# Kernel optimization log

Hardware: AMD Instinct MI355X
Metric: run time of the kernel (lower is better)

Reference implementation:

```python
import jax, jax.numpy as jnp
import numpy as np

MODEL_DIM = 256
NUM_HEADS = 4
HEAD_DIM = MODEL_DIM // NUM_HEADS
MAX_LEN = 512
EPS = 1e-5


def positional_embedding(n, dim):
    pos = jnp.arange(n, dtype=jnp.float32)[:, None]
    div = jnp.exp(jnp.arange(0, dim, 2, dtype=jnp.float32) * (-np.log(10000.0) / dim))
    pe = jnp.zeros((n, dim), dtype=jnp.float32)
    pe = pe.at[:, 0::2].set(jnp.sin(pos * div))
    pe = pe.at[:, 1::2].set(jnp.cos(pos * div))
    return pe


def layer_norm(x, g, b):
    mu = jnp.mean(x, axis=-1, keepdims=True)
    var = jnp.mean(jnp.square(x - mu), axis=-1, keepdims=True)
    return (x - mu) * jax.lax.rsqrt(var + EPS) * g + b


def setup_inputs() -> dict:
    key = jax.random.key(0)
    ks = jax.random.split(key, 20)
    B, N = 64, 512
    d = MODEL_DIM

    def lin(k, fan_in, fan_out):
        lim = 1.0 / np.sqrt(fan_in)
        return jax.random.uniform(k, (fan_out, fan_in), jnp.float32, -lim, lim)

    def xavier(k, fan_in, fan_out):
        lim = np.sqrt(6.0 / (fan_in + fan_out))
        return jax.random.uniform(k, (fan_out, fan_in), jnp.float32, -lim, lim)

    return {
        "x": jax.random.normal(ks[0], (B, N, 769), jnp.float32),
        "y": jax.random.normal(ks[1], (B, N, 674), jnp.float32),
        "z": jnp.zeros((B, 1), jnp.float32),
        "Wr": lin(ks[2], 769, d), "br": jnp.zeros((d,), jnp.float32),
        "Wf": lin(ks[3], 674, d), "bf": jnp.zeros((d,), jnp.float32),
        "g_x": jnp.ones((d,), jnp.float32), "b_x": jnp.zeros((d,), jnp.float32),
        "g_y": jnp.ones((d,), jnp.float32), "b_y": jnp.zeros((d,), jnp.float32),
        "Wq": xavier(ks[4], d, d), "bq": jnp.zeros((d,), jnp.float32),
        "Wk": xavier(ks[5], d, d), "bk": jnp.zeros((d,), jnp.float32),
        "Wv": xavier(ks[6], d, d), "bv": jnp.zeros((d,), jnp.float32),
        "Wo": xavier(ks[7], d, d), "bo": jnp.zeros((d,), jnp.float32),
        "g_m": jnp.ones((d,), jnp.float32), "b_m": jnp.zeros((d,), jnp.float32),
        "W1": lin(ks[8], d, d), "b1": jnp.zeros((d,), jnp.float32),
        "W2": lin(ks[9], d, d), "b2": jnp.zeros((d,), jnp.float32),
        "Wc": lin(ks[10], d, 2), "bc": jnp.zeros((2,), jnp.float32),
    }


def reference(x, y, z, Wr, br, Wf, bf, g_x, b_x, g_y, b_y,
              Wq, bq, Wk, bk, Wv, bv, Wo, bo, g_m, b_m,
              W1, b1, W2, b2, Wc, bc):
    B, N, _ = x.shape
    d, H, hd = MODEL_DIM, NUM_HEADS, HEAD_DIM
    pe = positional_embedding(MAX_LEN, d)[:N]  # (N, d)

    xp = layer_norm(x @ Wr.T + br + pe[None], g_x, b_x)  # (B,N,d)
    yp = layer_norm(y @ Wf.T + bf + pe[None], g_y, b_y)

    # cross-attention (non-causal, no masks, eval-mode dropout)
    q = (xp @ Wq.T + bq).reshape(B, N, H, hd)
    k = (yp @ Wk.T + bk).reshape(B, N, H, hd)
    v = (yp @ Wv.T + bv).reshape(B, N, H, hd)
    scale = hd ** -0.5
    scores = jnp.einsum("bshd,bthd->bhst", q, k) * scale  # (B,H,N,N)
    attn = jax.nn.softmax(scores, axis=-1)
    ctx = jnp.einsum("bhst,bthd->bshd", attn, v).reshape(B, N, d)
    attn_out = ctx @ Wo.T + bo

    x_res = layer_norm(xp + attn_out, g_m, b_m)
    mlp = jax.nn.relu(x_res @ W1.T + b1) @ W2.T + b2
    x_mlp = x_res + mlp
    pooled = jnp.mean(x_mlp, axis=1)  # (B,d)
    logits = pooled @ Wc.T + bc  # (B,2)
    return logits
```

## Files before the change

### kernel.cpp

```cpp
#include <hip/hip_runtime.h>
#include <hip/hip_bf16.h>

#define B_   64
#define N_   512
#define D_   256
#define H_   4
#define HD_  64

typedef __hip_bfloat16 bf16;
typedef __attribute__((ext_vector_type(8))) short short8;
typedef __attribute__((ext_vector_type(4))) float floatx4;

__device__ __forceinline__ float bf2f(bf16 v) { return __bfloat162float(v); }
__device__ __forceinline__ unsigned short f2us(float f) {
    bf16 h = __float2bfloat16(f);
    union { bf16 h; unsigned short u; } c; c.h = h; return c.u;
}

typedef __attribute__((address_space(1))) const unsigned int asg_u32;
typedef __attribute__((address_space(3))) unsigned int asl_u32;
__device__ __forceinline__ void gl_lds16(const void* g, void* l) {
    __builtin_amdgcn_global_load_lds((asg_u32*)g, (asl_u32*)l, 16, 0, 0);
}

__global__ __launch_bounds__(256)
void convw_k(const float* __restrict__ Wr, const float* __restrict__ Wf,
             const float* __restrict__ Wq, const float* __restrict__ Wk,
             const float* __restrict__ Wv, const float* __restrict__ Wo,
             const float* __restrict__ W1, const float* __restrict__ W2,
             bf16* __restrict__ dst)
{
    const int seg = blockIdx.y;
    const float* src; int Kreal, Kp; size_t off;
    switch (seg) {
        case 0: src = Wr; Kreal = 769; Kp = 800; off = 0; break;
        case 1: src = Wf; Kreal = 674; Kp = 704; off = 256 * 800; break;
        default:
            src = (seg == 2) ? Wq : (seg == 3) ? Wk : (seg == 4) ? Wv
                : (seg == 5) ? Wo : (seg == 6) ? W1 : W2;
            Kreal = 256; Kp = 256;
            off = 256 * 800 + 256 * 704 + (size_t)(seg - 2) * 256 * 256;
            break;
    }
    const int idx = blockIdx.x * 256 + threadIdx.x;
    if (idx >= 256 * Kp / 8) return;
    const int rowk = idx * 8;
    const int n = rowk / Kp, k0 = rowk % Kp;
    unsigned short tmp[8];
    #pragma unroll
    for (int j = 0; j < 8; ++j) {
        int kk = k0 + j;
        tmp[j] = f2us(kk < Kreal ? src[(size_t)n * Kreal + kk] : 0.f);
    }
    *(short8*)&dst[off + (size_t)rowk] = *(short8*)tmp;
}

__global__ __launch_bounds__(256)
void pe_k(float* __restrict__ pe)
{
    const int n = blockIdx.x, c = threadIdx.x;
    const int j = c & ~1;
    float freq = __expf(-(float)j * (9.210340371976184f / 256.0f));
    float ang = (float)n * freq;
    pe[n * 256 + c] = (c & 1) ? cosf(ang) : sinf(ang);
}

template<bool F32A>
__global__ __launch_bounds__(256)
void gemm_rp_t(const bf16* __restrict__ A, const float* __restrict__ A32,
               int lda, int Kreal,
               const bf16* __restrict__ W, int ldw,
               const float* __restrict__ bias, const bf16* __restrict__ res,
               const float* __restrict__ pe,
               const float* __restrict__ g, const float* __restrict__ bln,
               bf16* __restrict__ C, float* __restrict__ pp,
               int Kp, int relu, int tv)
{
    __shared__ bf16 As[2][4 * 64 * 8];
    __shared__ bf16 Bs[2][4 * 256 * 8];
    __shared__ float s_mu[64][4], s_sq[64][4];

    const int tid = threadIdx.x;
    const int m0 = blockIdx.x * 64;
    const int lane = tid & 63, w = tid >> 6;
    const int fr = lane & 15, quad = lane >> 4;

    const unsigned short* Wp = (const unsigned short*)W + (size_t)lane * ldw + w * 8;

    floatx4 acc[4][4] = {};
    int cur = 0;

    if constexpr (F32A) {
        const int srow = tid >> 2, skb = tid & 3;
        const float* a32p = A32 + (size_t)(m0 + srow) * Kreal + skb * 8;
        float av[8];
        #pragma unroll
        for (int j = 0; j < 8; ++j) {
            int kk = skb * 8 + j;
            av[j] = (kk < Kreal) ? a32p[j] : 0.f;
        }
        #pragma unroll
        for (int i = 0; i < 4; ++i)
            gl_lds16(Wp + (size_t)(i * 64) * ldw, &Bs[0][(w * 256 + i * 64 + lane) * 8]);

        for (int k0 = 0; k0 < Kp; k0 += 32) {
            __syncthreads();
            unsigned short uw[8];
            #pragma unroll
            for (int j = 0; j < 8; ++j) uw[j] = f2us(av[j]);
            *(short8*)&As[0][(skb * 64 + srow) * 8] = *(short8*)uw;
            __syncthreads();
            if (k0 + 32 < Kp) {
                const int nb = cur ^ 1;
                #pragma unroll
                for (int i = 0; i < 4; ++i)
                    gl_lds16(Wp + (size_t)(i * 64) * ldw + k0 + 32,
                             &Bs[nb][(w * 256 + i * 64 + lane) * 8]);
                #pragma unroll
                for (int j = 0; j < 8; ++j) {
                    int kk = k0 + 32 + skb * 8 + j;
                    av[j] = (kk < Kreal) ? a32p[k0 + 32 + j] : 0.f;
                }
            }
            short8 a[4];
            #pragma unroll
            for (int im = 0; im < 4; ++im)
                a[im] = *(const short8*)&As[0][(quad * 64 + im * 16 + fr) * 8];
            #pragma unroll
            for (int in = 0; in < 4; ++in) {
                short8 bfrag = *(const short8*)&Bs[cur][(quad * 256 + w * 64 + in * 16 + fr) * 8];
                #pragma unroll
                for (int im = 0; im < 4; ++im)
                    acc[im][in] = __builtin_amdgcn_mfma_f32_16x16x32_bf16(
                        a[im], bfrag, acc[im][in], 0, 0, 0);
            }
            cur ^= 1;
        }
    } else {
        const unsigned short* Ap = (const unsigned short*)A + (size_t)(m0 + lane) * lda + w * 8;
        gl_lds16(Ap, &As[0][(w * 64 + lane) * 8]);
        #pragma unroll
        for (int i = 0; i < 4; ++i)
            gl_lds16(Wp + (size_t)(i * 64) * ldw, &Bs[0][(w * 256 + i * 64 + lane) * 8]);

        for (int k0 = 0; k0 < Kp; k0 += 32) {
            __syncthreads();
            if (k0 + 32 < Kp) {
                const int nb = cur ^ 1;
                gl_lds16(Ap + k0 + 32, &As[nb][(w * 64 + lane) * 8]);
                #pragma unroll
                for (int i = 0; i < 4; ++i)
                    gl_lds16(Wp + (size_t)(i * 64) * ldw + k0 + 32,
                             &Bs[nb][(w * 256 + i * 64 + lane) * 8]);
            }
            short8 a[4];
            #pragma unroll
            for (int im = 0; im < 4; ++im)
                a[im] = *(const short8*)&As[cur][(quad * 64 + im * 16 + fr) * 8];
            #pragma unroll
            for (int in = 0; in < 4; ++in) {
                short8 bfrag = *(const short8*)&Bs[cur][(quad * 256 + w * 64 + in * 16 + fr) * 8];
                #pragma unroll
                for (int im = 0; im < 4; ++im)
                    acc[im][in] = __builtin_amdgcn_mfma_f32_16x16x32_bf16(
                        a[im], bfrag, acc[im][in], 0, 0, 0);
            }
            cur ^= 1;
        }
    }

    #pragma unroll
    for (int in = 0; in < 4; ++in) {
        const int n = w * 64 + in * 16 + fr;
        const float bi = bias[n];
        #pragma unroll
        for (int im = 0; im < 4; ++im) {
            #pragma unroll
            for (int reg = 0; reg < 4; ++reg) {
                const int m = m0 + im * 16 + quad * 4 + reg;
                float v = acc[im][in][reg] + bi;
                if (pe)   v += pe[((m & (N_ - 1)) << 8) + n];
                if (relu) v = fmaxf(v, 0.f);
                if (res)  v += bf2f(res[((size_t)m << 8) + n]);
                acc[im][in][reg] = v;
            }
        }
    }

    if (g) {
        #pragma unroll
        for (int im = 0; im < 4; ++im) {
            #pragma unroll
            for (int reg = 0; reg < 4; ++reg) {
                float ps = acc[im][0][reg] + acc[im][1][reg]
                         + acc[im][2][reg] + acc[im][3][reg];
                float pq = acc[im][0][reg] * acc[im][0][reg]
                         + acc[im][1][reg] * acc[im][1][reg]
                         + acc[im][2][reg] * acc[im][2][reg]
                         + acc[im][3][reg] * acc[im][3][reg];
                #pragma unroll
                for (int off = 1; off < 16; off <<= 1) {
                    ps += __shfl_xor(ps, off, 64);
                    pq += __shfl_xor(pq, off, 64);
                }
                if (fr == 0) {
                    const int r = im * 16 + quad * 4 + reg;
                    s_mu[r][w] = ps;
                    s_sq[r][w] = pq;
                }
            }
        }
        __syncthreads();
        #pragma unroll
        for (int im = 0; im < 4; ++im) {
            #pragma unroll
            for (int reg = 0; reg < 4; ++reg) {
                const int r = im * 16 + quad * 4 + reg;
                const float mu = (s_mu[r][0] + s_mu[r][1] + s_mu[r][2] + s_mu[r][3])
                                 * (1.f / 256.f);
                const float var = (s_sq[r][0] + s_sq[r][1] + s_sq[r][2] + s_sq[r][3])
                                  * (1.f / 256.f) - mu * mu;
                const float rs = rsqrtf(var + 1e-5f);
                const int m = m0 + r;
                #pragma unroll
                for (int in = 0; in < 4; ++in) {
                    const int n = w * 64 + in * 16 + fr;
                    C[((size_t)m << 8) + n] = __float2bfloat16(
                        (acc[im][in][reg] - mu) * rs * g[n] + bln[n]);
                }
            }
        }
    } else if (tv) {
        const int bh = ((m0 >> 9) << 2) + w;
        const int nn = m0 & (N_ - 1);
        unsigned short* Ct = (unsigned short*)C;
        #pragma unroll
        for (int in = 0; in < 4; ++in) {
            const int d = in * 16 + fr;
            #pragma unroll
            for (int im = 0; im < 4; ++im) {
                unsigned short pk[4];
                #pragma unroll
                for (int reg = 0; reg < 4; ++reg) pk[reg] = f2us(acc[im][in][reg]);
                *(ushort4*)&Ct[((size_t)(bh * 64 + d) << 9) + nn + im * 16 + quad * 4]
                    = *(ushort4*)pk;
            }
        }
    } else {
        #pragma unroll
        for (int im = 0; im < 4; ++im) {
            #pragma unroll
            for (int reg = 0; reg < 4; ++reg) {
                const int m = m0 + im * 16 + quad * 4 + reg;
                #pragma unroll
                for (int in = 0; in < 4; ++in) {
                    const int n = w * 64 + in * 16 + fr;
                    C[((size_t)m << 8) + n] = __float2bfloat16(acc[im][in][reg]);
                }
            }
        }
        if (pp) {
            #pragma unroll
            for (int in = 0; in < 4; ++in) {
                float s = 0.f;
                #pragma unroll
                for (int im = 0; im < 4; ++im)
                    #pragma unroll
                    for (int reg = 0; reg < 4; ++reg) s += acc[im][in][reg];
                s += __shfl_xor(s, 16, 64);
                s += __shfl_xor(s, 32, 64);
                if (quad == 0)
                    pp[((m0 >> 6) << 8) + w * 64 + in * 16 + fr] = s;
            }
        }
    }
}

__global__ __launch_bounds__(256)
void attn_k(const bf16* q, const bf16* __restrict__ k,
            const bf16* __restrict__ vt, bf16* ctx)
{
    __shared__ bf16 Ks[8 * 64 * 8];
    __shared__ bf16 Vs[8 * 64 * 8];
    __shared__ bf16 Ps[4 * 16 * 72];

    const int bid = blockIdx.x;
    const int l = (bid & 7) * 256 + (bid >> 3);
    const int qt = l & 7;
    const int h  = (l >> 3) & 3;
    const int b  = l >> 5;
    const int q0 = qt * 64;
    const size_t base  = ((size_t)b * N_) * D_ + h * HD_;
    const size_t vbase = ((size_t)(b * H_ + h) * HD_) * N_;

    const int tid = threadIdx.x;
    const int lane = tid & 63;
    const int w = tid >> 6;
    const int fr = lane & 15, quad = lane >> 4;

    short8 aq[2];
    #pragma unroll
    for (int ks = 0; ks < 2; ++ks)
        aq[ks] = *(const short8*)((const unsigned short*)q + base
                   + (size_t)(q0 + w * 16 + fr) * D_ + (ks * 4 + quad) * 8);

    floatx4 O[4] = {};
    float mrun[4], lrun[4];
    #pragma unroll
    for (int r = 0; r < 4; ++r) { mrun[r] = -1e30f; lrun[r] = 0.f; }

    const int srow = tid >> 2, sc = tid & 3;
    const unsigned short* kp = (const unsigned short*)k + base + (size_t)srow * D_ + sc * 16;
    const unsigned short* vp = (const unsigned short*)vt + vbase + (size_t)srow * N_ + sc * 16;
    const float C1 = 0.125f * 1.44269504f;

    for (int kt = 0; kt < 8; ++kt) {
        __syncthreads();
        {
            const unsigned short* srck = kp + (size_t)(kt * 64) * D_;
            *(short8*)&Ks[((sc * 2 + 0) * 64 + srow) * 8] = *(const short8*)(srck);
            *(short8*)&Ks[((sc * 2 + 1) * 64 + srow) * 8] = *(const short8*)(srck + 8);
            const unsigned short* srcv = vp + kt * 64;
            *(short8*)&Vs[((sc * 2 + 0) * 64 + srow) * 8] = *(const short8*)(srcv);
            *(short8*)&Vs[((sc * 2 + 1) * 64 + srow) * 8] = *(const short8*)(srcv + 8);
        }
        __syncthreads();

        floatx4 S[4] = {};
        __builtin_amdgcn_s_setprio(1);
        #pragma unroll
        for (int in = 0; in < 4; ++in) {
            #pragma unroll
            for (int ks = 0; ks < 2; ++ks) {
                short8 bk = *(const short8*)&Ks[((ks * 4 + quad) * 64 + in * 16 + fr) * 8];
                S[in] = __builtin_amdgcn_mfma_f32_16x16x32_bf16(aq[ks], bk, S[in], 0, 0, 0);
            }
        }
        __builtin_amdgcn_s_setprio(0);

        #pragma unroll
        for (int r = 0; r < 4; ++r) {
            float mloc = fmaxf(fmaxf(S[0][r], S[1][r]), fmaxf(S[2][r], S[3][r]));
            #pragma unroll
            for (int off = 1; off < 16; off <<= 1) mloc = fmaxf(mloc, __shfl_xor(mloc, off, 64));
            float mnew = fmaxf(mrun[r], mloc);
            float mc = mnew * C1;
            float alpha = exp2f(mrun[r] * C1 - mc);
            float rs = 0.f;
            #pragma unroll
            for (int in = 0; in < 4; ++in) {
                float p = exp2f(S[in][r] * C1 - mc);
                S[in][r] = p;
                rs += p;
            }
            #pragma unroll
            for (int off = 1; off < 16; off <<= 1) rs += __shfl_xor(rs, off, 64);
            lrun[r] = lrun[r] * alpha + rs;
            mrun[r] = mnew;
            #pragma unroll
            for (int in = 0; in < 4; ++in) O[in][r] *= alpha;
        }

        #pragma unroll
        for (int in = 0; in < 4; ++in)
            #pragma unroll
            for (int r = 0; r < 4; ++r)
                Ps[(w * 16 + quad * 4 + r) * 72 + in * 16 + fr] = __float2bfloat16(S[in][r]);
        short8 pa[2];
        #pragma unroll
        for (int ks = 0; ks < 2; ++ks)
            pa[ks] = *(const short8*)&Ps[(w * 16 + fr) * 72 + ks * 32 + quad * 8];

        __builtin_amdgcn_s_setprio(1);
        #pragma unroll
        for (int in = 0; in < 4; ++in) {
            #pragma unroll
            for (int ks = 0; ks < 2; ++ks) {
                short8 bv = *(const short8*)&Vs[((ks * 4 + quad) * 64 + in * 16 + fr) * 8];
                O[in] = __builtin_amdgcn_mfma_f32_16x16x32_bf16(pa[ks], bv, O[in], 0, 0, 0);
            }
        }
        __builtin_amdgcn_s_setprio(0);
    }

    #pragma unroll
    for (int r = 0; r < 4; ++r) {
        const float inv = 1.f / lrun[r];
        const int row = q0 + w * 16 + quad * 4 + r;
        #pragma unroll
        for (int in = 0; in < 4; ++in)
            ctx[base + (size_t)row * D_ + in * 16 + fr] = __float2bfloat16(O[in][r] * inv);
    }
}

__global__ __launch_bounds__(256)
void logits_k(const float* __restrict__ partial, const float* __restrict__ Wc,
              const float* __restrict__ bc, float* __restrict__ out)
{
    __shared__ float pl[256];
    __shared__ float red[256];
    int b = blockIdx.x, c = threadIdx.x;
    float s = 0.f;
    for (int ch = 0; ch < 8; ++ch) s += partial[((size_t)b * 8 + ch) * D_ + c];
    pl[c] = s * (1.f / 512.f);
    __syncthreads();
    int o = c >> 7, cc = c & 127;
    red[c] = pl[cc] * Wc[o * 256 + cc] + pl[cc + 128] * Wc[o * 256 + cc + 128];
    __syncthreads();
    for (int st = 64; st > 0; st >>= 1) { if (cc < st) red[c] += red[c + st]; __syncthreads(); }
    if (cc == 0) out[b * 2 + o] = red[c] + bc[o];
}

extern "C" void kernel_launch(void* const* d_in, const int* in_sizes, int n_in,
                              void* d_out, int out_size, void* d_ws, size_t ws_size,
                              hipStream_t stream)
{
    const float* x   = (const float*)d_in[0];
    const float* y   = (const float*)d_in[1];
    const float* Wr  = (const float*)d_in[3];
    const float* br  = (const float*)d_in[4];
    const float* Wf  = (const float*)d_in[5];
    const float* bfv = (const float*)d_in[6];
    const float* gx  = (const float*)d_in[7];
    const float* bx  = (const float*)d_in[8];
    const float* gy  = (const float*)d_in[9];
    const float* by  = (const float*)d_in[10];
    const float* Wq  = (const float*)d_in[11];
    const float* bq  = (const float*)d_in[12];
    const float* Wk  = (const float*)d_in[13];
    const float* bk  = (const float*)d_in[14];
    const float* Wv  = (const float*)d_in[15];
    const float* bv  = (const float*)d_in[16];
    const float* Wo  = (const float*)d_in[17];
    const float* bo  = (const float*)d_in[18];
    const float* gm  = (const float*)d_in[19];
    const float* bm  = (const float*)d_in[20];
    const float* W1  = (const float*)d_in[21];
    const float* b1  = (const float*)d_in[22];
    const float* W2  = (const float*)d_in[23];
    const float* b2  = (const float*)d_in[24];
    const float* Wc  = (const float*)d_in[25];
    const float* bc  = (const float*)d_in[26];

    bf16* ws = (bf16*)d_ws;
    const size_t S = (size_t)B_ * N_ * D_;
    bf16*  wb   = ws;
    float* pe   = (float*)(ws + 778240);
    float* part = pe + 131072;
    bf16*  bA   = ws + 778240 + 4 * 131072;
    bf16*  bB   = bA + S;
    bf16*  bC   = bB + S;
    bf16*  bD   = bC + S;
    bf16*  bE   = bD + S;

    bf16* Wrb = wb;
    bf16* Wfb = wb + 256 * 800;
    bf16* Wqb = Wfb + 256 * 704;
    bf16* Wkb = Wqb + 65536;
    bf16* Wvb = Wkb + 65536;
    bf16* Wob = Wvb + 65536;
    bf16* W1b = Wob + 65536;
    bf16* W2b = W1b + 65536;

    const int M = B_ * N_;
    dim3 blk(256);
    dim3 grp(M / 64);

    pe_k<<<N_, blk, 0, stream>>>(pe);
    convw_k<<<dim3(100, 8), blk, 0, stream>>>(Wr, Wf, Wq, Wk, Wv, Wo, W1, W2, wb);

    gemm_rp_t<true><<<grp, blk, 0, stream>>>(nullptr, x, 0, 769, Wrb, 800,
        br, nullptr, pe, gx, bx, bA, nullptr, 800, 0, 0);
    gemm_rp_t<true><<<grp, blk, 0, stream>>>(nullptr, y, 0, 674, Wfb, 704,
        bfv, nullptr, pe, gy, by, bB, nullptr, 704, 0, 0);
    gemm_rp_t<false><<<grp, blk, 0, stream>>>(bA, nullptr, 256, 256, Wqb, 256,
        bq, nullptr, nullptr, nullptr, nullptr, bC, nullptr, 256, 0, 0);
    gemm_rp_t<false><<<grp, blk, 0, stream>>>(bB, nullptr, 256, 256, Wkb, 256,
        bk, nullptr, nullptr, nullptr, nullptr, bD, nullptr, 256, 0, 0);
    gemm_rp_t<false><<<grp, blk, 0, stream>>>(bB, nullptr, 256, 256, Wvb, 256,
        bv, nullptr, nullptr, nullptr, nullptr, bE, nullptr, 256, 0, 1);
    attn_k<<<B_ * H_ * 8, blk, 0, stream>>>(bC, bD, bE, bC);
    gemm_rp_t<false><<<grp, blk, 0, stream>>>(bC, nullptr, 256, 256, Wob, 256,
        bo, bA, nullptr, gm, bm, bD, nullptr, 256, 0, 0);
    gemm_rp_t<false><<<grp, blk, 0, stream>>>(bD, nullptr, 256, 256, W1b, 256,
        b1, nullptr, nullptr, nullptr, nullptr, bE, nullptr, 256, 1, 0);
    gemm_rp_t<false><<<grp, blk, 0, stream>>>(bE, nullptr, 256, 256, W2b, 256,
        b2, bD, nullptr, nullptr, nullptr, bB, part, 256, 0, 0);
    logits_k<<<B_, blk, 0, stream>>>(part, Wc, bc, (float*)d_out);
}
```

Before: 569.7 us.

## Halve GEMM row tile to 32 and software-pipeline fp32 A loads into LDS

Shrinks the fused GEMM M tile from 64 to 32 rows, doubling the grid to 1024 blocks so more CUs stay busy and per-thread accumulators drop. The fp32 input path now converts the next tile's A into the alternate LDS buffer before compute, which removes one barrier per k-step, and loads are split into 4-wide chunks. The per-block partial pooling sums double to 16 per batch, and the workspace is resized to hold them. The cost is that each block re-reads the full weight tile for half as many rows, doubling weight traffic from L2.

```diff
diff --git a/kernel.cpp b/kernel.cpp
--- a/kernel.cpp
+++ b/kernel.cpp
@@ -76,92 +76,127 @@
                bf16* __restrict__ C, float* __restrict__ pp,
                int Kp, int relu, int tv)
 {
-    __shared__ bf16 As[2][4 * 64 * 8];
+    __shared__ bf16 As[2][4 * 32 * 8];
     __shared__ bf16 Bs[2][4 * 256 * 8];
-    __shared__ float s_mu[64][4], s_sq[64][4];
+    __shared__ float s_mu[32][4], s_sq[32][4];
 
     const int tid = threadIdx.x;
-    const int m0 = blockIdx.x * 64;
+    const int m0 = blockIdx.x * 32;
     const int lane = tid & 63, w = tid >> 6;
     const int fr = lane & 15, quad = lane >> 4;
+    const int nt = Kp / 32;
 
     const unsigned short* Wp = (const unsigned short*)W + (size_t)lane * ldw + w * 8;
 
-    floatx4 acc[4][4] = {};
+    floatx4 acc[2][4] = {};
     int cur = 0;
 
     if constexpr (F32A) {
-        const int srow = tid >> 2, skb = tid & 3;
-        const float* a32p = A32 + (size_t)(m0 + srow) * Kreal + skb * 8;
-        float av[8];
-        #pragma unroll
-        for (int j = 0; j < 8; ++j) {
-            int kk = skb * 8 + j;
-            av[j] = (kk < Kreal) ? a32p[j] : 0.f;
-        }
+        const int srow = (tid >> 3) & 31;
+        const int ksub = tid & 7;
+        const int g4 = ksub >> 1;
+        const int sub = (ksub & 1) * 4;
+        const float* a32p = A32 + (size_t)(m0 + srow) * Kreal + ksub * 4;
+        float av[4];
+
+        #pragma unroll
+        for (int j = 0; j < 4; ++j) av[j] = a32p[j];
         #pragma unroll
         for (int i = 0; i < 4; ++i)
             gl_lds16(Wp + (size_t)(i * 64) * ldw, &Bs[0][(w * 256 + i * 64 + lane) * 8]);
-
-        for (int k0 = 0; k0 < Kp; k0 += 32) {
+        {
+            unsigned short uw[4];
+            #pragma unroll
+            for (int j = 0; j < 4; ++j) uw[j] = f2us(av[j]);
+            *(ushort4*)&As[0][(g4 * 32 + srow) * 8 + sub] = *(ushort4*)uw;
+        }
+        if (nt > 1) {
+            const int kL = 32;
+            if (kL + 32 <= Kreal) {
+                #pragma unroll
+                for (int j = 0; j < 4; ++j) av[j] = a32p[kL + j];
+            } else {
+                #pragma unroll
+                for (int j = 0; j < 4; ++j) {
+                    int kk = kL + ksub * 4 + j;
+                    av[j] = (kk < Kreal) ? a32p[kL + j] : 0.f;
+                }
+            }
+        }
+
+        for (int t = 0; t < nt; ++t) {
             __syncthreads();
-            unsigned short uw[8];
-            #pragma unroll
-            for (int j = 0; j < 8; ++j) uw[j] = f2us(av[j]);
-            *(short8*)&As[0][(skb * 64 + srow) * 8] = *(short8*)uw;
-            __syncthreads();
-            if (k0 + 32 < Kp) {
-                const int nb = cur ^ 1;
+            const int nb = cur ^ 1;
+            if (t + 1 < nt) {
+                const int kB = (t + 1) * 32;
                 #pragma unroll
                 for (int i = 0; i < 4; ++i)
-                    gl_lds16(Wp + (size_t)(i * 64) * ldw + k0 + 32,
+                    gl_lds16(Wp + (size_t)(i * 64) * ldw + kB,
                              &Bs[nb][(w * 256 + i * 64 + lane) * 8]);
-                #pragma unroll
-                for (int j = 0; j < 8; ++j) {
-                    int kk = k0 + 32 + skb * 8 + j;
-                    av[j] = (kk < Kreal) ? a32p[k0 + 32 + j] : 0.f;
+                unsigned short uw[4];
+                #pragma unroll
+                for (int j = 0; j < 4; ++j) uw[j] = f2us(av[j]);
+                *(ushort4*)&As[nb][(g4 * 32 + srow) * 8 + sub] = *(ushort4*)uw;
+                if (t + 2 < nt) {
+                    const int kL = (t + 2) * 32;
+                    if (kL + 32 <= Kreal) {
+                        #pragma unroll
+                        for (int j = 0; j < 4; ++j) av[j] = a32p[kL + j];
+                    } else {
+                        #pragma unroll
+                        for (int j = 0; j < 4; ++j) {
+                            int kk = kL + ksub * 4 + j;
+                            av[j] = (kk < Kreal) ? a32p[kL + j] : 0.f;
+                        }
+                    }
                 }
             }
-            short8 a[4];
-            #pragma unroll
-            for (int im = 0; im < 4; ++im)
-                a[im] = *(const short8*)&As[0][(quad * 64 + im * 16 + fr) * 8];
+            short8 a[2];
+            #pragma unroll
+            for (int im = 0; im < 2; ++im)
+                a[im] = *(const short8*)&As[cur][(quad * 32 + im * 16 + fr) * 8];
             #pragma unroll
             for (int in = 0; in < 4; ++in) {
                 short8 bfrag = *(const short8*)&Bs[cur][(quad * 256 + w * 64 + in * 16 + fr) * 8];
                 #pragma unroll
-                for (int im = 0; im < 4; ++im)
+                for (int im = 0; im < 2; ++im)
                     acc[im][in] = __builtin_amdgcn_mfma_f32_16x16x32_bf16(
                         a[im], bfrag, acc[im][in], 0, 0, 0);
             }
             cur ^= 1;
         }
     } else {
-        const unsigned short* Ap = (const unsigned short*)A + (size_t)(m0 + lane) * lda + w * 8;
-        gl_lds16(Ap, &As[0][(w * 64 + lane) * 8]);
+        const int arow = lane & 31, ag = (w & 1) * 2 + (lane >> 5);
+        const bool doA = (w < 2);
+        const unsigned short* Ap = (const unsigned short*)A + (size_t)(m0 + arow) * lda + ag * 8;
+        bf16* AsD0 = &As[0][(ag * 32 + arow) * 8];
+        bf16* AsD1 = &As[1][(ag * 32 + arow) * 8];
+
+        if (doA) gl_lds16(Ap, AsD0);
         #pragma unroll
         for (int i = 0; i < 4; ++i)
             gl_lds16(Wp + (size_t)(i * 64) * ldw, &Bs[0][(w * 256 + i * 64 + lane) * 8]);
 
-        for (int k0 = 0; k0 < Kp; k0 += 32) {
+        for (int t = 0; t < nt; ++t) {
             __syncthreads();
-            if (k0 + 32 < Kp) {
-                const int nb = cur ^ 1;
-                gl_lds16(Ap + k0 + 32, &As[nb][(w * 64 + lane) * 8]);
+            const int nb = cur ^ 1;
+            if (t + 1 < nt) {
+                const int kB = (t + 1) * 32;
+                if (doA) gl_lds16(Ap + kB, nb ? AsD1 : AsD0);
                 #pragma unroll
                 for (int i = 0; i < 4; ++i)
-                    gl_lds16(Wp + (size_t)(i * 64) * ldw + k0 + 32,
+                    gl_lds16(Wp + (size_t)(i * 64) * ldw + kB,
                              &Bs[nb][(w * 256 + i * 64 + lane) * 8]);
             }
-            short8 a[4];
-            #pragma unroll
-            for (int im = 0; im < 4; ++im)
-                a[im] = *(const short8*)&As[cur][(quad * 64 + im * 16 + fr) * 8];
+            short8 a[2];
+            #pragma unroll
+            for (int im = 0; im < 2; ++im)
+                a[im] = *(const short8*)&As[cur][(quad * 32 + im * 16 + fr) * 8];
             #pragma unroll
             for (int in = 0; in < 4; ++in) {
                 short8 bfrag = *(const short8*)&Bs[cur][(quad * 256 + w * 64 + in * 16 + fr) * 8];
                 #pragma unroll
-                for (int im = 0; im < 4; ++im)
+                for (int im = 0; im < 2; ++im)
                     acc[im][in] = __builtin_amdgcn_mfma_f32_16x16x32_bf16(
                         a[im], bfrag, acc[im][in], 0, 0, 0);
             }
@@ -174,7 +209,7 @@
         const int n = w * 64 + in * 16 + fr;
         const float bi = bias[n];
         #pragma unroll
-        for (int im = 0; im < 4; ++im) {
+        for (int im = 0; im < 2; ++im) {
             #pragma unroll
             for (int reg = 0; reg < 4; ++reg) {
                 const int m = m0 + im * 16 + quad * 4 + reg;
@@ -189,7 +224,7 @@
 
     if (g) {
         #pragma unroll
-        for (int im = 0; im < 4; ++im) {
+        for (int im = 0; im < 2; ++im) {
             #pragma unroll
             for (int reg = 0; reg < 4; ++reg) {
                 float ps = acc[im][0][reg] + acc[im][1][reg]
@@ -212,7 +247,7 @@
         }
         __syncthreads();
         #pragma unroll
-        for (int im = 0; im < 4; ++im) {
+        for (int im = 0; im < 2; ++im) {
             #pragma unroll
             for (int reg = 0; reg < 4; ++reg) {
                 const int r = im * 16 + quad * 4 + reg;
@@ -238,7 +273,7 @@
         for (int in = 0; in < 4; ++in) {
             const int d = in * 16 + fr;
             #pragma unroll
-            for (int im = 0; im < 4; ++im) {
+            for (int im = 0; im < 2; ++im) {
                 unsigned short pk[4];
                 #pragma unroll
                 for (int reg = 0; reg < 4; ++reg) pk[reg] = f2us(acc[im][in][reg]);
@@ -248,7 +283,7 @@
         }
     } else {
         #pragma unroll
-        for (int im = 0; im < 4; ++im) {
+        for (int im = 0; im < 2; ++im) {
             #pragma unroll
             for (int reg = 0; reg < 4; ++reg) {
                 const int m = m0 + im * 16 + quad * 4 + reg;
@@ -264,13 +299,13 @@
             for (int in = 0; in < 4; ++in) {
                 float s = 0.f;
                 #pragma unroll
-                for (int im = 0; im < 4; ++im)
+                for (int im = 0; im < 2; ++im)
                     #pragma unroll
                     for (int reg = 0; reg < 4; ++reg) s += acc[im][in][reg];
                 s += __shfl_xor(s, 16, 64);
                 s += __shfl_xor(s, 32, 64);
                 if (quad == 0)
-                    pp[((m0 >> 6) << 8) + w * 64 + in * 16 + fr] = s;
+                    pp[(size_t)blockIdx.x * 256 + w * 64 + in * 16 + fr] = s;
             }
         }
     }
@@ -401,7 +436,7 @@
     __shared__ float red[256];
     int b = blockIdx.x, c = threadIdx.x;
     float s = 0.f;
-    for (int ch = 0; ch < 8; ++ch) s += partial[((size_t)b * 8 + ch) * D_ + c];
+    for (int ch = 0; ch < 16; ++ch) s += partial[((size_t)b * 16 + ch) * D_ + c];
     pl[c] = s * (1.f / 512.f);
     __syncthreads();
     int o = c >> 7, cc = c & 127;
@@ -447,7 +482,7 @@
     bf16*  wb   = ws;
     float* pe   = (float*)(ws + 778240);
     float* part = pe + 131072;
-    bf16*  bA   = ws + 778240 + 4 * 131072;
+    bf16*  bA   = ws + 778240 + 6 * 131072;
     bf16*  bB   = bA + S;
     bf16*  bC   = bB + S;
     bf16*  bD   = bC + S;
@@ -464,7 +499,7 @@
 
     const int M = B_ * N_;
     dim3 blk(256);
-    dim3 grp(M / 64);
+    dim3 grp(M / 32);
 
     pe_k<<<N_, blk, 0, stream>>>(pe);
     convw_k<<<dim3(100, 8), blk, 0, stream>>>(Wr, Wf, Wq, Wk, Wv, Wo, W1, W2, wb);
```

New measurement: 669.9 us. 1.18x slower.

## Triple-buffer GEMM K-loop with explicit vmcnt waits and single barrier

Applied to the files above, without the earlier changes.

Moves the row-projection GEMM's K loop from double to triple buffering in LDS, issuing loads two stages ahead. Explicit s_waitcnt vmcnt counts and one raw s_barrier per step replace the paired __syncthreads. The fp32-A path now holds two register stages, alternating between them via a lambda, and converts to bf16 one stage ahead. The goal is to hide global-load latency and cut barrier stalls, at the cost of more LDS (lower occupancy) and fragile hand-tuned wait counts.

```diff
diff --git a/kernel.cpp b/kernel.cpp
--- a/kernel.cpp
+++ b/kernel.cpp
@@ -22,6 +22,13 @@
 __device__ __forceinline__ void gl_lds16(const void* g, void* l) {
     __builtin_amdgcn_global_load_lds((asg_u32*)g, (asl_u32*)l, 16, 0, 0);
 }
+
+__device__ __forceinline__ void wait_vm12() { asm volatile("s_waitcnt vmcnt(12)" ::: "memory"); }
+__device__ __forceinline__ void wait_vm5()  { asm volatile("s_waitcnt vmcnt(5)"  ::: "memory"); }
+__device__ __forceinline__ void wait_vm0()  { asm volatile("s_waitcnt vmcnt(0)"  ::: "memory"); }
+__device__ __forceinline__ void wait_lg0()  { asm volatile("s_waitcnt lgkmcnt(0)" ::: "memory"); }
+__device__ __forceinline__ void bar()       { __builtin_amdgcn_s_barrier(); }
+__device__ __forceinline__ void schedb()    { __builtin_amdgcn_sched_barrier(0); }
 
 __global__ __launch_bounds__(256)
 void convw_k(const float* __restrict__ Wr, const float* __restrict__ Wf,
@@ -76,96 +83,130 @@
                bf16* __restrict__ C, float* __restrict__ pp,
                int Kp, int relu, int tv)
 {
-    __shared__ bf16 As[2][4 * 64 * 8];
-    __shared__ bf16 Bs[2][4 * 256 * 8];
+    __shared__ bf16 As[3][4 * 64 * 8];
+    __shared__ bf16 Bs[3][4 * 256 * 8];
     __shared__ float s_mu[64][4], s_sq[64][4];
 
     const int tid = threadIdx.x;
     const int m0 = blockIdx.x * 64;
     const int lane = tid & 63, w = tid >> 6;
     const int fr = lane & 15, quad = lane >> 4;
+    const int nt = Kp / 32;
 
     const unsigned short* Wp = (const unsigned short*)W + (size_t)lane * ldw + w * 8;
 
     floatx4 acc[4][4] = {};
-    int cur = 0;
+    int rb = 0, w1 = 1, w2 = 2;
 
     if constexpr (F32A) {
-        const int srow = tid >> 2, skb = tid & 3;
-        const float* a32p = A32 + (size_t)(m0 + srow) * Kreal + skb * 8;
-        float av[8];
-        #pragma unroll
-        for (int j = 0; j < 8; ++j) {
-            int kk = skb * 8 + j;
-            av[j] = (kk < Kreal) ? a32p[j] : 0.f;
-        }
+        const int srow = tid >> 2, skb = tid & 3, kb8 = skb * 8;
+        const float* a32p = A32 + (size_t)(m0 + srow) * Kreal + kb8;
+        float avA[8], avB[8];
+
+        #pragma unroll
+        for (int j = 0; j < 8; ++j) avA[j] = a32p[j];
         #pragma unroll
         for (int i = 0; i < 4; ++i)
             gl_lds16(Wp + (size_t)(i * 64) * ldw, &Bs[0][(w * 256 + i * 64 + lane) * 8]);
-
-        for (int k0 = 0; k0 < Kp; k0 += 32) {
-            __syncthreads();
+        {
             unsigned short uw[8];
             #pragma unroll
-            for (int j = 0; j < 8; ++j) uw[j] = f2us(av[j]);
+            for (int j = 0; j < 8; ++j) uw[j] = f2us(avA[j]);
             *(short8*)&As[0][(skb * 64 + srow) * 8] = *(short8*)uw;
-            __syncthreads();
-            if (k0 + 32 < Kp) {
-                const int nb = cur ^ 1;
+        }
+        #pragma unroll
+        for (int j = 0; j < 8; ++j) avB[j] = a32p[32 + j];
+        #pragma unroll
+        for (int i = 0; i < 4; ++i)
+            gl_lds16(Wp + (size_t)(i * 64) * ldw + 32, &Bs[1][(w * 256 + i * 64 + lane) * 8]);
+
+        auto f32a_step = [&](int t_, float (&AVC)[8], float (&AVN)[8]) {
+            if (t_ + 1 < nt) { wait_vm12(); } else { wait_vm0(); }
+            wait_lg0();
+            bar();
+            schedb();
+            if (t_ + 2 < nt) {
+                const int kL = (t_ + 2) * 32;
+                if (kL + 32 <= Kreal) {
+                    #pragma unroll
+                    for (int j = 0; j < 8; ++j) AVN[j] = a32p[kL + j];
+                } else {
+                    #pragma unroll
+                    for (int j = 0; j < 8; ++j) {
+                        int kk = kL + kb8 + j;
+                        int offv = (kk < Kreal) ? (kL + j) : 0;
+                        float tvv = a32p[offv];
+                        AVN[j] = (kk < Kreal) ? tvv : 0.f;
+                    }
+                }
                 #pragma unroll
                 for (int i = 0; i < 4; ++i)
-                    gl_lds16(Wp + (size_t)(i * 64) * ldw + k0 + 32,
-                             &Bs[nb][(w * 256 + i * 64 + lane) * 8]);
-                #pragma unroll
-                for (int j = 0; j < 8; ++j) {
-                    int kk = k0 + 32 + skb * 8 + j;
-                    av[j] = (kk < Kreal) ? a32p[k0 + 32 + j] : 0.f;
-                }
-            }
+                    gl_lds16(Wp + (size_t)(i * 64) * ldw + kL,
+                             &Bs[w2][(w * 256 + i * 64 + lane) * 8]);
+            }
+            if (t_ + 1 < nt) {
+                unsigned short uw[8];
+                #pragma unroll
+                for (int j = 0; j < 8; ++j) uw[j] = f2us(AVC[j]);
+                *(short8*)&As[w1][(skb * 64 + srow) * 8] = *(short8*)uw;
+            }
+            schedb();
             short8 a[4];
             #pragma unroll
             for (int im = 0; im < 4; ++im)
-                a[im] = *(const short8*)&As[0][(quad * 64 + im * 16 + fr) * 8];
+                a[im] = *(const short8*)&As[rb][(quad * 64 + im * 16 + fr) * 8];
             #pragma unroll
             for (int in = 0; in < 4; ++in) {
-                short8 bfrag = *(const short8*)&Bs[cur][(quad * 256 + w * 64 + in * 16 + fr) * 8];
+                short8 bfrag = *(const short8*)&Bs[rb][(quad * 256 + w * 64 + in * 16 + fr) * 8];
                 #pragma unroll
                 for (int im = 0; im < 4; ++im)
                     acc[im][in] = __builtin_amdgcn_mfma_f32_16x16x32_bf16(
                         a[im], bfrag, acc[im][in], 0, 0, 0);
             }
-            cur ^= 1;
+            int tmp_ = rb; rb = w1; w1 = w2; w2 = tmp_;
+        };
+        for (int t = 0; t < nt; t += 2) {
+            f32a_step(t, avB, avA);
+            if (t + 1 < nt) f32a_step(t + 1, avA, avB);
         }
     } else {
         const unsigned short* Ap = (const unsigned short*)A + (size_t)(m0 + lane) * lda + w * 8;
+
         gl_lds16(Ap, &As[0][(w * 64 + lane) * 8]);
         #pragma unroll
         for (int i = 0; i < 4; ++i)
             gl_lds16(Wp + (size_t)(i * 64) * ldw, &Bs[0][(w * 256 + i * 64 + lane) * 8]);
-
-        for (int k0 = 0; k0 < Kp; k0 += 32) {
-            __syncthreads();
-            if (k0 + 32 < Kp) {
-                const int nb = cur ^ 1;
-                gl_lds16(Ap + k0 + 32, &As[nb][(w * 64 + lane) * 8]);
+        gl_lds16(Ap + 32, &As[1][(w * 64 + lane) * 8]);
+        #pragma unroll
+        for (int i = 0; i < 4; ++i)
+            gl_lds16(Wp + (size_t)(i * 64) * ldw + 32, &Bs[1][(w * 256 + i * 64 + lane) * 8]);
+
+        for (int t = 0; t < nt; ++t) {
+            if (t + 1 < nt) { wait_vm5(); } else { wait_vm0(); }
+            bar();
+            schedb();
+            if (t + 2 < nt) {
+                const int kB = (t + 2) * 32;
+                gl_lds16(Ap + kB, &As[w2][(w * 64 + lane) * 8]);
                 #pragma unroll
                 for (int i = 0; i < 4; ++i)
-                    gl_lds16(Wp + (size_t)(i * 64) * ldw + k0 + 32,
-                             &Bs[nb][(w * 256 + i * 64 + lane) * 8]);
-            }
+                    gl_lds16(Wp + (size_t)(i * 64) * ldw + kB,
+                             &Bs[w2][(w * 256 + i * 64 + lane) * 8]);
+            }
+            schedb();
             short8 a[4];
             #pragma unroll
             for (int im = 0; im < 4; ++im)
-                a[im] = *(const short8*)&As[cur][(quad * 64 + im * 16 + fr) * 8];
+                a[im] = *(const short8*)&As[rb][(quad * 64 + im * 16 + fr) * 8];
             #pragma unroll
             for (int in = 0; in < 4; ++in) {
-                short8 bfrag = *(const short8*)&Bs[cur][(quad * 256 + w * 64 + in * 16 + fr) * 8];
+                short8 bfrag = *(const short8*)&Bs[rb][(quad * 256 + w * 64 + in * 16 + fr) * 8];
                 #pragma unroll
                 for (int im = 0; im < 4; ++im)
                     acc[im][in] = __builtin_amdgcn_mfma_f32_16x16x32_bf16(
                         a[im], bfrag, acc[im][in], 0, 0, 0);
             }
-            cur ^= 1;
+            int tmp_ = rb; rb = w1; w1 = w2; w2 = tmp_;
         }
     }
 
```

New measurement: 549.9 us. -3.5%, faster.

## Load GEMM operand fragments directly from global memory into registers, bypassing LDS

Applied to the files above, without the earlier changes.

Rewrites the row-panel GEMM so each wave loads its MFMA A and B fragments straight from global memory into registers. Loads are double-buffered in registers, so the LDS staging buffers and per-iteration barriers go away. Blocks grow to 512 threads (8 waves, 2 row halves by 4 column quarters), which halves each wave's accumulator tile and changes the pooled partial-sum layout to 16 chunks per batch. The risk is that the per-lane strided global loads are less coalesced and reuse across waves now depends on the cache instead of LDS.

```diff
diff --git a/kernel.cpp b/kernel.cpp
--- a/kernel.cpp
+++ b/kernel.cpp
@@ -15,12 +15,6 @@
 __device__ __forceinline__ unsigned short f2us(float f) {
     bf16 h = __float2bfloat16(f);
     union { bf16 h; unsigned short u; } c; c.h = h; return c.u;
-}
-
-typedef __attribute__((address_space(1))) const unsigned int asg_u32;
-typedef __attribute__((address_space(3))) unsigned int asl_u32;
-__device__ __forceinline__ void gl_lds16(const void* g, void* l) {
-    __builtin_amdgcn_global_load_lds((asg_u32*)g, (asl_u32*)l, 16, 0, 0);
 }
 
 __global__ __launch_bounds__(256)
@@ -66,118 +60,121 @@
 }
 
 template<bool F32A>
-__global__ __launch_bounds__(256)
-void gemm_rp_t(const bf16* __restrict__ A, const float* __restrict__ A32,
-               int lda, int Kreal,
-               const bf16* __restrict__ W, int ldw,
-               const float* __restrict__ bias, const bf16* __restrict__ res,
-               const float* __restrict__ pe,
-               const float* __restrict__ g, const float* __restrict__ bln,
-               bf16* __restrict__ C, float* __restrict__ pp,
-               int Kp, int relu, int tv)
-{
-    __shared__ bf16 As[2][4 * 64 * 8];
-    __shared__ bf16 Bs[2][4 * 256 * 8];
+__global__ __launch_bounds__(512, 4)
+void gemm_df(const bf16* __restrict__ A, const float* __restrict__ A32,
+             int lda, int Kreal,
+             const bf16* __restrict__ W, int ldw,
+             const float* __restrict__ bias, const bf16* __restrict__ res,
+             const float* __restrict__ pe,
+             const float* __restrict__ g, const float* __restrict__ bln,
+             bf16* __restrict__ C, float* __restrict__ pp,
+             int Kp, int relu, int tv)
+{
     __shared__ float s_mu[64][4], s_sq[64][4];
 
     const int tid = threadIdx.x;
     const int m0 = blockIdx.x * 64;
     const int lane = tid & 63, w = tid >> 6;
+    const int rh = w & 1;
+    const int cq = w >> 1;
     const int fr = lane & 15, quad = lane >> 4;
-
-    const unsigned short* Wp = (const unsigned short*)W + (size_t)lane * ldw + w * 8;
-
-    floatx4 acc[4][4] = {};
-    int cur = 0;
+    const int nt = Kp / 32;
+
+    const unsigned short* wp = (const unsigned short*)W
+        + (size_t)(cq * 64 + fr) * ldw + quad * 8;
+    const float* ap32 = F32A
+        ? A32 + (size_t)(m0 + rh * 32 + fr) * Kreal + quad * 8 : nullptr;
+    const unsigned short* apb = F32A ? nullptr
+        : (const unsigned short*)A + (size_t)(m0 + rh * 32 + fr) * lda + quad * 8;
+
+    floatx4 acc[2][4] = {};
+
+    auto ldB = [&](int t, short8 (&fb)[4]) {
+        const int k0 = t * 32;
+        #pragma unroll
+        for (int in = 0; in < 4; ++in)
+            fb[in] = *(const short8*)(wp + (size_t)(in * 16) * ldw + k0);
+    };
+    auto step = [&](short8 (&a)[2], short8 (&b)[4]) {
+        #pragma unroll
+        for (int in = 0; in < 4; ++in)
+            #pragma unroll
+            for (int im = 0; im < 2; ++im)
+                acc[im][in] = __builtin_amdgcn_mfma_f32_16x16x32_bf16(
+                    a[im], b[in], acc[im][in], 0, 0, 0);
+    };
 
     if constexpr (F32A) {
-        const int srow = tid >> 2, skb = tid & 3;
-        const float* a32p = A32 + (size_t)(m0 + srow) * Kreal + skb * 8;
-        float av[8];
-        #pragma unroll
-        for (int j = 0; j < 8; ++j) {
-            int kk = skb * 8 + j;
-            av[j] = (kk < Kreal) ? a32p[j] : 0.f;
-        }
-        #pragma unroll
-        for (int i = 0; i < 4; ++i)
-            gl_lds16(Wp + (size_t)(i * 64) * ldw, &Bs[0][(w * 256 + i * 64 + lane) * 8]);
-
-        for (int k0 = 0; k0 < Kp; k0 += 32) {
-            __syncthreads();
-            unsigned short uw[8];
-            #pragma unroll
-            for (int j = 0; j < 8; ++j) uw[j] = f2us(av[j]);
-            *(short8*)&As[0][(skb * 64 + srow) * 8] = *(short8*)uw;
-            __syncthreads();
-            if (k0 + 32 < Kp) {
-                const int nb = cur ^ 1;
-                #pragma unroll
-                for (int i = 0; i < 4; ++i)
-                    gl_lds16(Wp + (size_t)(i * 64) * ldw + k0 + 32,
-                             &Bs[nb][(w * 256 + i * 64 + lane) * 8]);
-                #pragma unroll
-                for (int j = 0; j < 8; ++j) {
-                    int kk = k0 + 32 + skb * 8 + j;
-                    av[j] = (kk < Kreal) ? a32p[k0 + 32 + j] : 0.f;
-                }
-            }
-            short8 a[4];
-            #pragma unroll
-            for (int im = 0; im < 4; ++im)
-                a[im] = *(const short8*)&As[0][(quad * 64 + im * 16 + fr) * 8];
-            #pragma unroll
-            for (int in = 0; in < 4; ++in) {
-                short8 bfrag = *(const short8*)&Bs[cur][(quad * 256 + w * 64 + in * 16 + fr) * 8];
-                #pragma unroll
-                for (int im = 0; im < 4; ++im)
-                    acc[im][in] = __builtin_amdgcn_mfma_f32_16x16x32_bf16(
-                        a[im], bfrag, acc[im][in], 0, 0, 0);
-            }
-            cur ^= 1;
+        auto ldA = [&](int t, float (&fa)[2][8]) {
+            const int k0 = t * 32;
+            if (k0 + 32 <= Kreal) {
+                #pragma unroll
+                for (int im = 0; im < 2; ++im)
+                    #pragma unroll
+                    for (int j = 0; j < 8; ++j)
+                        fa[im][j] = ap32[(size_t)(im * 16) * Kreal + k0 + j];
+            } else {
+                #pragma unroll
+                for (int im = 0; im < 2; ++im)
+                    #pragma unroll
+                    for (int j = 0; j < 8; ++j) {
+                        const int kk = k0 + quad * 8 + j;
+                        fa[im][j] = (kk < Kreal)
+                            ? ap32[(size_t)(im * 16) * Kreal + k0 + j] : 0.f;
+                    }
+            }
+        };
+        auto cvt2 = [&](float (&fa)[2][8], short8 (&pa)[2]) {
+            #pragma unroll
+            for (int im = 0; im < 2; ++im) {
+                unsigned short uw[8];
+                #pragma unroll
+                for (int j = 0; j < 8; ++j) uw[j] = f2us(fa[im][j]);
+                pa[im] = *(short8*)uw;
+            }
+        };
+
+        float faA[2][8], faB[2][8];
+        short8 fbA[4], fbB[4];
+        ldA(0, faA); ldB(0, fbA);
+        for (int t = 0; t < nt; t += 2) {
+            if (t + 1 < nt) { ldA(t + 1, faB); ldB(t + 1, fbB); }
+            short8 pa[2]; cvt2(faA, pa);
+            step(pa, fbA);
+            if (t + 1 < nt) {
+                if (t + 2 < nt) { ldA(t + 2, faA); ldB(t + 2, fbA); }
+                short8 pb[2]; cvt2(faB, pb);
+                step(pb, fbB);
+            }
         }
     } else {
-        const unsigned short* Ap = (const unsigned short*)A + (size_t)(m0 + lane) * lda + w * 8;
-        gl_lds16(Ap, &As[0][(w * 64 + lane) * 8]);
-        #pragma unroll
-        for (int i = 0; i < 4; ++i)
-            gl_lds16(Wp + (size_t)(i * 64) * ldw, &Bs[0][(w * 256 + i * 64 + lane) * 8]);
-
-        for (int k0 = 0; k0 < Kp; k0 += 32) {
-            __syncthreads();
-            if (k0 + 32 < Kp) {
-                const int nb = cur ^ 1;
-                gl_lds16(Ap + k0 + 32, &As[nb][(w * 64 + lane) * 8]);
-                #pragma unroll
-                for (int i = 0; i < 4; ++i)
-                    gl_lds16(Wp + (size_t)(i * 64) * ldw + k0 + 32,
-                             &Bs[nb][(w * 256 + i * 64 + lane) * 8]);
-            }
-            short8 a[4];
-            #pragma unroll
-            for (int im = 0; im < 4; ++im)
-                a[im] = *(const short8*)&As[cur][(quad * 64 + im * 16 + fr) * 8];
-            #pragma unroll
-            for (int in = 0; in < 4; ++in) {
-                short8 bfrag = *(const short8*)&Bs[cur][(quad * 256 + w * 64 + in * 16 + fr) * 8];
-                #pragma unroll
-                for (int im = 0; im < 4; ++im)
-                    acc[im][in] = __builtin_amdgcn_mfma_f32_16x16x32_bf16(
-                        a[im], bfrag, acc[im][in], 0, 0, 0);
-            }
-            cur ^= 1;
+        auto ldAb = [&](int t, short8 (&fa)[2]) {
+            const int k0 = t * 32;
+            #pragma unroll
+            for (int im = 0; im < 2; ++im)
+                fa[im] = *(const short8*)(apb + (size_t)(im * 16) * lda + k0);
+        };
+        short8 faA[2], faB[2], fbA[4], fbB[4];
+        ldAb(0, faA); ldB(0, fbA);
+        for (int t = 0; t < nt; t += 2) {
+            if (t + 1 < nt) { ldAb(t + 1, faB); ldB(t + 1, fbB); }
+            step(faA, fbA);
+            if (t + 1 < nt) {
+                if (t + 2 < nt) { ldAb(t + 2, faA); ldB(t + 2, fbA); }
+                step(faB, fbB);
+            }
         }
     }
 
     #pragma unroll
     for (int in = 0; in < 4; ++in) {
-        const int n = w * 64 + in * 16 + fr;
+        const int n = cq * 64 + in * 16 + fr;
         const float bi = bias[n];
         #pragma unroll
-        for (int im = 0; im < 4; ++im) {
+        for (int im = 0; im < 2; ++im) {
             #pragma unroll
             for (int reg = 0; reg < 4; ++reg) {
-                const int m = m0 + im * 16 + quad * 4 + reg;
+                const int m = m0 + rh * 32 + im * 16 + quad * 4 + reg;
                 float v = acc[im][in][reg] + bi;
                 if (pe)   v += pe[((m & (N_ - 1)) << 8) + n];
                 if (relu) v = fmaxf(v, 0.f);
@@ -189,7 +186,7 @@
 
     if (g) {
         #pragma unroll
-        for (int im = 0; im < 4; ++im) {
+        for (int im = 0; im < 2; ++im) {
             #pragma unroll
             for (int reg = 0; reg < 4; ++reg) {
                 float ps = acc[im][0][reg] + acc[im][1][reg]
@@ -204,18 +201,18 @@
                     pq += __shfl_xor(pq, off, 64);
                 }
                 if (fr == 0) {
-                    const int r = im * 16 + quad * 4 + reg;
-                    s_mu[r][w] = ps;
-                    s_sq[r][w] = pq;
+                    const int r = rh * 32 + im * 16 + quad * 4 + reg;
+                    s_mu[r][cq] = ps;
+                    s_sq[r][cq] = pq;
                 }
             }
         }
         __syncthreads();
         #pragma unroll
-        for (int im = 0; im < 4; ++im) {
+        for (int im = 0; im < 2; ++im) {
             #pragma unroll
             for (int reg = 0; reg < 4; ++reg) {
-                const int r = im * 16 + quad * 4 + reg;
+                const int r = rh * 32 + im * 16 + quad * 4 + reg;
                 const float mu = (s_mu[r][0] + s_mu[r][1] + s_mu[r][2] + s_mu[r][3])
                                  * (1.f / 256.f);
                 const float var = (s_sq[r][0] + s_sq[r][1] + s_sq[r][2] + s_sq[r][3])
@@ -224,21 +221,21 @@
                 const int m = m0 + r;
                 #pragma unroll
                 for (int in = 0; in < 4; ++in) {
-                    const int n = w * 64 + in * 16 + fr;
+                    const int n = cq * 64 + in * 16 + fr;
                     C[((size_t)m << 8) + n] = __float2bfloat16(
                         (acc[im][in][reg] - mu) * rs * g[n] + bln[n]);
                 }
             }
         }
     } else if (tv) {
-        const int bh = ((m0 >> 9) << 2) + w;
-        const int nn = m0 & (N_ - 1);
+        const int bh = ((m0 >> 9) << 2) + cq;
+        const int nn = (m0 & (N_ - 1)) + rh * 32;
         unsigned short* Ct = (unsigned short*)C;
         #pragma unroll
         for (int in = 0; in < 4; ++in) {
             const int d = in * 16 + fr;
             #pragma unroll
-            for (int im = 0; im < 4; ++im) {
+            for (int im = 0; im < 2; ++im) {
                 unsigned short pk[4];
                 #pragma unroll
                 for (int reg = 0; reg < 4; ++reg) pk[reg] = f2us(acc[im][in][reg]);
@@ -248,13 +245,13 @@
         }
     } else {
         #pragma unroll
-        for (int im = 0; im < 4; ++im) {
+        for (int im = 0; im < 2; ++im) {
             #pragma unroll
             for (int reg = 0; reg < 4; ++reg) {
-                const int m = m0 + im * 16 + quad * 4 + reg;
+                const int m = m0 + rh * 32 + im * 16 + quad * 4 + reg;
                 #pragma unroll
                 for (int in = 0; in < 4; ++in) {
-                    const int n = w * 64 + in * 16 + fr;
+                    const int n = cq * 64 + in * 16 + fr;
                     C[((size_t)m << 8) + n] = __float2bfloat16(acc[im][in][reg]);
                 }
             }
@@ -264,13 +261,13 @@
             for (int in = 0; in < 4; ++in) {
                 float s = 0.f;
                 #pragma unroll
-                for (int im = 0; im < 4; ++im)
+                for (int im = 0; im < 2; ++im)
                     #pragma unroll
                     for (int reg = 0; reg < 4; ++reg) s += acc[im][in][reg];
                 s += __shfl_xor(s, 16, 64);
                 s += __shfl_xor(s, 32, 64);
                 if (quad == 0)
-                    pp[((m0 >> 6) << 8) + w * 64 + in * 16 + fr] = s;
+                    pp[(size_t)(blockIdx.x * 2 + rh) * 256 + cq * 64 + in * 16 + fr] = s;
             }
         }
     }
@@ -401,7 +398,7 @@
     __shared__ float red[256];
     int b = blockIdx.x, c = threadIdx.x;
     float s = 0.f;
-    for (int ch = 0; ch < 8; ++ch) s += partial[((size_t)b * 8 + ch) * D_ + c];
+    for (int ch = 0; ch < 16; ++ch) s += partial[((size_t)b * 16 + ch) * D_ + c];
     pl[c] = s * (1.f / 512.f);
     __syncthreads();
     int o = c >> 7, cc = c & 127;
@@ -447,7 +444,7 @@
     bf16*  wb   = ws;
     float* pe   = (float*)(ws + 778240);
     float* part = pe + 131072;
-    bf16*  bA   = ws + 778240 + 4 * 131072;
+    bf16*  bA   = ws + 778240 + 6 * 131072;
     bf16*  bB   = bA + S;
     bf16*  bC   = bB + S;
     bf16*  bD   = bC + S;
@@ -464,27 +461,28 @@
 
     const int M = B_ * N_;
     dim3 blk(256);
+    dim3 blk512(512);
     dim3 grp(M / 64);
 
     pe_k<<<N_, blk, 0, stream>>>(pe);
     convw_k<<<dim3(100, 8), blk, 0, stream>>>(Wr, Wf, Wq, Wk, Wv, Wo, W1, W2, wb);
 
-    gemm_rp_t<true><<<grp, blk, 0, stream>>>(nullptr, x, 0, 769, Wrb, 800,
+    gemm_df<true><<<grp, blk512, 0, stream>>>(nullptr, x, 0, 769, Wrb, 800,
         br, nullptr, pe, gx, bx, bA, nullptr, 800, 0, 0);
-    gemm_rp_t<true><<<grp, blk, 0, stream>>>(nullptr, y, 0, 674, Wfb, 704,
+    gemm_df<true><<<grp, blk512, 0, stream>>>(nullptr, y, 0, 674, Wfb, 704,
         bfv, nullptr, pe, gy, by, bB, nullptr, 704, 0, 0);
-    gemm_rp_t<false><<<grp, blk, 0, stream>>>(bA, nullptr, 256, 256, Wqb, 256,
+    gemm_df<false><<<grp, blk512, 0, stream>>>(bA, nullptr, 256, 256, Wqb, 256,
         bq, nullptr, nullptr, nullptr, nullptr, bC, nullptr, 256, 0, 0);
-    gemm_rp_t<false><<<grp, blk, 0, stream>>>(bB, nullptr, 256, 256, Wkb, 256,
+    gemm_df<false><<<grp, blk512, 0, stream>>>(bB, nullptr, 256, 256, Wkb, 256,
         bk, nullptr, nullptr, nullptr, nullptr, bD, nullptr, 256, 0, 0);
-    gemm_rp_t<false><<<grp, blk, 0, stream>>>(bB, nullptr, 256, 256, Wvb, 256,
+    gemm_df<false><<<grp, blk512, 0, stream>>>(bB, nullptr, 256, 256, Wvb, 256,
         bv, nullptr, nullptr, nullptr, nullptr, bE, nullptr, 256, 0, 1);
     attn_k<<<B_ * H_ * 8, blk, 0, stream>>>(bC, bD, bE, bC);
-    gemm_rp_t<false><<<grp, blk, 0, stream>>>(bC, nullptr, 256, 256, Wob, 256,
+    gemm_df<false><<<grp, blk512, 0, stream>>>(bC, nullptr, 256, 256, Wob, 256,
         bo, bA, nullptr, gm, bm, bD, nullptr, 256, 0, 0);
-    gemm_rp_t<false><<<grp, blk, 0, stream>>>(bD, nullptr, 256, 256, W1b, 256,
+    gemm_df<false><<<grp, blk512, 0, stream>>>(bD, nullptr, 256, 256, W1b, 256,
         b1, nullptr, nullptr, nullptr, nullptr, bE, nullptr, 256, 1, 0);
-    gemm_rp_t<false><<<grp, blk, 0, stream>>>(bE, nullptr, 256, 256, W2b, 256,
+    gemm_df<false><<<grp, blk512, 0, stream>>>(bE, nullptr, 256, 256, W2b, 256,
         b2, bD, nullptr, nullptr, nullptr, bB, part, 256, 0, 0);
     logits_k<<<B_, blk, 0, stream>>>(part, Wc, bc, (float*)d_out);
 }
```

After: 644.4 us. 1.13x slower.
